# Kernel optimization log

Measured on AMD Instinct MI355X. Metric: run time of the kernel, lower is better.

The kernel has to match this reference:

```python
import jax, jax.numpy as jnp
import numpy as np

B, N, DIM = 1, 4096, 1024
HEADS, DIM_HEAD = 12, 8
POST_LOG_SCALE = 1.0
SCALE = DIM_HEAD ** -0.5


def setup_inputs() -> dict:
    key = jax.random.key(0)
    kx, kw = jax.random.split(key)
    x = jax.random.normal(kx, (B, N, DIM), dtype=jnp.float32)
    # torch nn.Linear(dim, heads*dim_head*2, bias=False) weight: [2*heads*dim_head, dim]
    W = jax.random.normal(kw, (2 * HEADS * DIM_HEAD, DIM), dtype=jnp.float32) * (DIM ** -0.5)
    return {"x": x, "W": W}


def reference(x, W):
    b, n, _ = x.shape
    # linear: x @ W^T -> [b, n, 2*h*d]; rearrange '(qk h d) -> qk b h n d'
    proj = jnp.einsum('bnc,oc->bno', x, W)
    proj = proj.reshape(b, n, 2, HEADS, DIM_HEAD)
    q = jnp.transpose(proj[:, :, 0], (0, 2, 1, 3))  # [b, h, n, d]
    k = jnp.transpose(proj[:, :, 1], (0, 2, 1, 3))  # [b, h, n, d]
    # small-d QK matmul -> [b, h, n, n]
    gates = jnp.einsum('bhid,bhjd->bhij', q, k) * SCALE
    gates = jax.nn.log_sigmoid(gates) * POST_LOG_SCALE
    # causal_mask = triu(ones, diagonal=0); masked_fill -> zero on/above diagonal
    i = jnp.arange(n)[:, None]
    j = jnp.arange(n)[None, :]
    keep = j < i  # strictly lower-triangular entries survive
    gates = jnp.where(keep, gates, 0.0)
    # flip-cumsum-flip == reverse cumulative sum along last axis
    gates = jax.lax.cumsum(gates, axis=3, reverse=True)
    return gates
```

## Files before the change

kernel.cpp:

```cpp
#include <hip/hip_runtime.h>

#define NTOK 4096
#define DIMC 1024
#define HEADS 12
#define DH 8
#define QSCALE 0.35355339059327373f
#define LOG2E  1.4426950408889634f
#define LN2    0.6931471805599453f
#define QPRE   (QSCALE * LOG2E)

typedef float f4 __attribute__((ext_vector_type(4)));
typedef float f2 __attribute__((ext_vector_type(2)));

#define KOFF (HEADS * NTOK * DH)

__global__ __launch_bounds__(256) void k1_proj(const float* __restrict__ x,
                                               const float* __restrict__ W,
                                               float* __restrict__ qk) {
    __shared__ float xs[8 * 1028];
    const int t = threadIdx.x;
    const int row0 = blockIdx.x * 8;

    const f4* x4 = (const f4*)(x + (size_t)row0 * DIMC);
    #pragma unroll
    for (int i = 0; i < 8; ++i) {
        int f = t + i * 256;
        int r = f >> 8;
        int c4 = f & 255;
        f4 v = x4[f];
        *(f4*)(&xs[r * 1028 + c4 * 4]) = v;
    }
    __syncthreads();

    const int g  = t >> 2;
    const int rg = t & 3;

    f2 acc[2][3];
    #pragma unroll
    for (int a = 0; a < 2; ++a)
        #pragma unroll
        for (int m = 0; m < 3; ++m) acc[a][m] = (f2)(0.f);

    const float* w0 = W + (size_t)(3 * g) * DIMC;
    #pragma unroll 2
    for (int c = 0; c < DIMC; c += 4) {
        f4 w[3];
        #pragma unroll
        for (int m = 0; m < 3; ++m)
            w[m] = *(const f4*)(w0 + (size_t)m * DIMC + c);
        #pragma unroll
        for (int a = 0; a < 2; ++a) {
            f4 xv = *(const f4*)(&xs[(rg * 2 + a) * 1028 + c]);
            #pragma unroll
            for (int m = 0; m < 3; ++m) {
                acc[a][m] = __builtin_elementwise_fma(xv.xy, w[m].xy, acc[a][m]);
                acc[a][m] = __builtin_elementwise_fma(xv.zw, w[m].zw, acc[a][m]);
            }
        }
    }

    #pragma unroll
    for (int m = 0; m < 3; ++m) {
        int o   = 3 * g + m;
        int qkf = (o >= 96) ? 1 : 0;
        int oo  = o - 96 * qkf;
        int h   = oo >> 3;
        int d   = oo & 7;
        #pragma unroll
        for (int a = 0; a < 2; ++a) {
            int n = row0 + rg * 2 + a;
            float v = acc[a][m].x + acc[a][m].y;
            if (!qkf) {
                qk[((size_t)h * NTOK + n) * DH + d] = v * QPRE;
            } else {
                qk[KOFF + (((size_t)h * 16 + (n >> 8)) * DH + d) * 256 + (n & 255)] = v;
            }
        }
    }
}

__device__ __forceinline__ float lsig2(float u) {
    float mn = fminf(u, 0.f);
    float z  = __builtin_amdgcn_exp2f(-fabsf(u));
    return mn - __builtin_amdgcn_logf(1.f + z);
}

__global__ __launch_bounds__(256) void k2_gates(const float* __restrict__ qk,
                                                float* __restrict__ out) {
    const int bid  = blockIdx.x;
    const int h    = bid >> 10;
    const int r0   = (bid & 1023) << 2;
    const int t    = threadIdx.x;
    const int lane = t & 63;
    const int w    = t >> 6;
    const int r    = r0 + w;

    __shared__ float ks[2][8 * 256];

    const float* qp = qk + ((size_t)h * NTOK + r) * DH;
    float qs[8];
    #pragma unroll
    for (int d = 0; d < 8; ++d) qs[d] = qp[d];

    float* o = out + ((size_t)h * NTOK + r) * NTOK;
    const int cb = r0 >> 8;
    const int rm = r & 255;

    f4 z = (f4)(0.f);
    for (int cc = 15; cc > cb; --cc)
        __builtin_nontemporal_store(z, (f4*)(o + cc * 256 + 4 * lane));

    {
        const float* kt = qk + KOFF + ((size_t)h * 16 + cb) * 2048;
        f4 a = *(const f4*)(kt + 4 * t);
        f4 b = *(const f4*)(kt + 4 * t + 1024);
        *(f4*)(&ks[0][4 * t]) = a;
        *(f4*)(&ks[0][4 * t + 1024]) = b;
    }
    __syncthreads();

    float carry = 0.f;
    int p = 0;

    for (int c = cb; c >= 0; --c) {
        const int cn = (c > 0) ? (c - 1) : 0;
        const float* kt = qk + KOFF + ((size_t)h * 16 + cn) * 2048;
        f4 sa = *(const f4*)(kt + 4 * t);
        f4 sb = *(const f4*)(kt + 4 * t + 1024);

        f4 kv[8];
        #pragma unroll
        for (int d = 0; d < 8; ++d)
            kv[d] = *(const f4*)(&ks[p][d * 256 + 4 * lane]);

        f2 A = (f2)(0.f), B = (f2)(0.f);
        #pragma unroll
        for (int d = 0; d < 8; ++d) {
            A = __builtin_elementwise_fma(kv[d].xy, (f2)(qs[d]), A);
            B = __builtin_elementwise_fma(kv[d].zw, (f2)(qs[d]), B);
        }

        float g[4];
        if (c == cb) {
            g[0] = (4 * lane + 0 < rm) ? lsig2(A.x) : 0.f;
            g[1] = (4 * lane + 1 < rm) ? lsig2(A.y) : 0.f;
            g[2] = (4 * lane + 2 < rm) ? lsig2(B.x) : 0.f;
            g[3] = (4 * lane + 3 < rm) ? lsig2(B.y) : 0.f;
        } else {
            g[0] = lsig2(A.x); g[1] = lsig2(A.y);
            g[2] = lsig2(B.x); g[3] = lsig2(B.y);
        }

        g[2] += g[3]; g[1] += g[2]; g[0] += g[1];
        const float tot = g[0];
        float s = tot;
        #pragma unroll
        for (int off = 1; off < 64; off <<= 1) {
            float v = __shfl_down(s, off, 64);
            if (lane + off < 64) s += v;
        }
        const float base = (s - tot) + carry;
        carry += __builtin_amdgcn_readfirstlane(s);

        f4 gv = {g[0], g[1], g[2], g[3]};
        __builtin_nontemporal_store((gv + base) * LN2, (f4*)(o + c * 256 + 4 * lane));

        *(f4*)(&ks[p ^ 1][4 * t]) = sa;
        *(f4*)(&ks[p ^ 1][4 * t + 1024]) = sb;
        __syncthreads();
        p ^= 1;
    }
}

extern "C" void kernel_launch(void* const* d_in, const int* in_sizes, int n_in,
                              void* d_out, int out_size, void* d_ws, size_t ws_size,
                              hipStream_t stream) {
    const float* x = (const float*)d_in[0];
    const float* W = (const float*)d_in[1];
    float* out = (float*)d_out;
    float* qk  = (float*)d_ws;

    hipLaunchKernelGGL(k1_proj, dim3(NTOK / 8), dim3(256), 0, stream, x, W, qk);
    hipLaunchKernelGGL(k2_gates, dim3(HEADS * NTOK / 4), dim3(256), 0, stream, qk, out);
}
```

Before: 201.2 us.

## Split gate kernel into segment-totals pass and per-segment scan with tiled stores

```diff
diff --git a/kernel.cpp b/kernel.cpp
--- a/kernel.cpp
+++ b/kernel.cpp
@@ -13,6 +13,7 @@
 typedef float f2 __attribute__((ext_vector_type(2)));
 
 #define KOFF (HEADS * NTOK * DH)
+#define TOFF (2 * KOFF)
 
 __global__ __launch_bounds__(256) void k1_proj(const float* __restrict__ x,
                                                const float* __restrict__ W,
@@ -85,90 +86,123 @@
     return mn - __builtin_amdgcn_logf(1.f + z);
 }
 
-__global__ __launch_bounds__(256) void k2_gates(const float* __restrict__ qk,
-                                                float* __restrict__ out) {
-    const int bid  = blockIdx.x;
-    const int h    = bid >> 10;
-    const int r0   = (bid & 1023) << 2;
+__global__ __launch_bounds__(256) void kA_totals(const float* __restrict__ qk,
+                                                 float* __restrict__ T) {
+    const int blk  = blockIdx.x;
+    const int h    = blk >> 6;
+    const int ib   = blk & 63;
     const int t    = threadIdx.x;
     const int lane = t & 63;
-    const int w    = t >> 6;
-    const int r    = r0 + w;
-
-    __shared__ float ks[2][8 * 256];
+    const int s    = t >> 6;
+    const int i    = ib * 64 + lane;
+
+    const float* qp = qk + ((size_t)h * NTOK + i) * DH;
+    float q[8];
+    #pragma unroll
+    for (int d = 0; d < 8; ++d) q[d] = qp[d];
+
+    float sum = 0.f;
+    const int jlo = s * 1024;
+    int jhi = ib * 64 + 63;
+    if (jhi > jlo + 1024) jhi = jlo + 1024;
+
+    if (jhi > jlo) {
+        for (int j0 = ((jhi - 1) & ~3); j0 >= jlo; j0 -= 4) {
+            const float* kt = qk + KOFF + ((size_t)h * 16 + (j0 >> 8)) * 2048 + (j0 & 255);
+            f2 A = (f2)(0.f), B = (f2)(0.f);
+            #pragma unroll
+            for (int d = 0; d < 8; ++d) {
+                f4 kv = *(const f4*)(kt + d * 256);
+                A = __builtin_elementwise_fma(kv.xy, (f2)(q[d]), A);
+                B = __builtin_elementwise_fma(kv.zw, (f2)(q[d]), B);
+            }
+            float g0 = (j0 + 0 < i) ? lsig2(A.x) : 0.f;
+            float g1 = (j0 + 1 < i) ? lsig2(A.y) : 0.f;
+            float g2 = (j0 + 2 < i) ? lsig2(B.x) : 0.f;
+            float g3 = (j0 + 3 < i) ? lsig2(B.y) : 0.f;
+            sum += g3; sum += g2; sum += g1; sum += g0;
+        }
+    }
+    T[TOFF - TOFF + ((size_t)h * 4 + s) * NTOK + i] = sum;
+}
+
+__global__ __launch_bounds__(64) void kB_gates(const float* __restrict__ qk,
+                                               const float* __restrict__ T,
+                                               float* __restrict__ out) {
+    const int blk  = blockIdx.x;
+    const int s    = blk & 3;
+    const int ib   = (blk >> 2) & 63;
+    const int h    = blk >> 8;
+    const int lane = threadIdx.x;
+    const int r    = ib * 64 + lane;
+
+    __shared__ float tile[64 * 68];
 
     const float* qp = qk + ((size_t)h * NTOK + r) * DH;
-    float qs[8];
-    #pragma unroll
-    for (int d = 0; d < 8; ++d) qs[d] = qp[d];
-
-    float* o = out + ((size_t)h * NTOK + r) * NTOK;
-    const int cb = r0 >> 8;
-    const int rm = r & 255;
-
-    f4 z = (f4)(0.f);
-    for (int cc = 15; cc > cb; --cc)
-        __builtin_nontemporal_store(z, (f4*)(o + cc * 256 + 4 * lane));
-
-    {
-        const float* kt = qk + KOFF + ((size_t)h * 16 + cb) * 2048;
-        f4 a = *(const f4*)(kt + 4 * t);
-        f4 b = *(const f4*)(kt + 4 * t + 1024);
-        *(f4*)(&ks[0][4 * t]) = a;
-        *(f4*)(&ks[0][4 * t + 1024]) = b;
-    }
-    __syncthreads();
+    float q[8];
+    #pragma unroll
+    for (int d = 0; d < 8; ++d) q[d] = qp[d];
 
     float carry = 0.f;
-    int p = 0;
-
-    for (int c = cb; c >= 0; --c) {
-        const int cn = (c > 0) ? (c - 1) : 0;
-        const float* kt = qk + KOFF + ((size_t)h * 16 + cn) * 2048;
-        f4 sa = *(const f4*)(kt + 4 * t);
-        f4 sb = *(const f4*)(kt + 4 * t + 1024);
-
-        f4 kv[8];
-        #pragma unroll
-        for (int d = 0; d < 8; ++d)
-            kv[d] = *(const f4*)(&ks[p][d * 256 + 4 * lane]);
-
-        f2 A = (f2)(0.f), B = (f2)(0.f);
-        #pragma unroll
-        for (int d = 0; d < 8; ++d) {
-            A = __builtin_elementwise_fma(kv[d].xy, (f2)(qs[d]), A);
-            B = __builtin_elementwise_fma(kv[d].zw, (f2)(qs[d]), B);
-        }
-
-        float g[4];
-        if (c == cb) {
-            g[0] = (4 * lane + 0 < rm) ? lsig2(A.x) : 0.f;
-            g[1] = (4 * lane + 1 < rm) ? lsig2(A.y) : 0.f;
-            g[2] = (4 * lane + 2 < rm) ? lsig2(B.x) : 0.f;
-            g[3] = (4 * lane + 3 < rm) ? lsig2(B.y) : 0.f;
+    #pragma unroll
+    for (int s2 = 3; s2 >= 1; --s2)
+        if (s2 > s) carry += T[((size_t)h * 4 + s2) * NTOK + r];
+
+    float* orow0 = out + ((size_t)h * NTOK + ib * 64) * NTOK;
+    const f4 z = (f4)(0.f);
+
+    for (int jb = s * 16 + 15; jb >= s * 16; --jb) {
+        if (jb > ib) {
+            #pragma unroll
+            for (int rr = 0; rr < 16; ++rr) {
+                int row = rr * 4 + (lane >> 4);
+                int c4  = (lane & 15) * 4;
+                __builtin_nontemporal_store(z,
+                    (f4*)(orow0 + (size_t)row * NTOK + jb * 64 + c4));
+            }
         } else {
-            g[0] = lsig2(A.x); g[1] = lsig2(A.y);
-            g[2] = lsig2(B.x); g[3] = lsig2(B.y);
-        }
-
-        g[2] += g[3]; g[1] += g[2]; g[0] += g[1];
-        const float tot = g[0];
-        float s = tot;
-        #pragma unroll
-        for (int off = 1; off < 64; off <<= 1) {
-            float v = __shfl_down(s, off, 64);
-            if (lane + off < 64) s += v;
-        }
-        const float base = (s - tot) + carry;
-        carry += __builtin_amdgcn_readfirstlane(s);
-
-        f4 gv = {g[0], g[1], g[2], g[3]};
-        __builtin_nontemporal_store((gv + base) * LN2, (f4*)(o + c * 256 + 4 * lane));
-
-        *(f4*)(&ks[p ^ 1][4 * t]) = sa;
-        *(f4*)(&ks[p ^ 1][4 * t + 1024]) = sb;
-        __syncthreads();
-        p ^= 1;
+            const bool diag = (jb == ib);
+            const float* kt = qk + KOFF + ((size_t)h * 16 + (jb >> 2)) * 2048 + (jb & 3) * 64;
+
+            for (int jf = 15; jf >= 0; --jf) {
+                const int j0 = jb * 64 + jf * 4;
+                const float* kp = kt + jf * 4;
+                f2 A = (f2)(0.f), B = (f2)(0.f);
+                #pragma unroll
+                for (int d = 0; d < 8; ++d) {
+                    f4 kv = *(const f4*)(kp + d * 256);
+                    A = __builtin_elementwise_fma(kv.xy, (f2)(q[d]), A);
+                    B = __builtin_elementwise_fma(kv.zw, (f2)(q[d]), B);
+                }
+                float g0, g1, g2, g3;
+                if (diag) {
+                    g0 = (j0 + 0 < r) ? lsig2(A.x) : 0.f;
+                    g1 = (j0 + 1 < r) ? lsig2(A.y) : 0.f;
+                    g2 = (j0 + 2 < r) ? lsig2(B.x) : 0.f;
+                    g3 = (j0 + 3 < r) ? lsig2(B.y) : 0.f;
+                } else {
+                    g0 = lsig2(A.x); g1 = lsig2(A.y);
+                    g2 = lsig2(B.x); g3 = lsig2(B.y);
+                }
+                float v3 = g3 + carry;
+                float v2 = g2 + v3;
+                float v1 = g1 + v2;
+                float v0 = g0 + v1;
+                carry = v0;
+                f4 v = {v0 * LN2, v1 * LN2, v2 * LN2, v3 * LN2};
+                *(f4*)(&tile[lane * 68 + jf * 4]) = v;
+            }
+            __syncthreads();
+            #pragma unroll
+            for (int rr = 0; rr < 16; ++rr) {
+                int row = rr * 4 + (lane >> 4);
+                int c4  = (lane & 15) * 4;
+                f4 v = *(const f4*)(&tile[row * 68 + c4]);
+                __builtin_nontemporal_store(v,
+                    (f4*)(orow0 + (size_t)row * NTOK + jb * 64 + c4));
+            }
+            __syncthreads();
+        }
     }
 }
 
@@ -179,7 +213,9 @@
     const float* W = (const float*)d_in[1];
     float* out = (float*)d_out;
     float* qk  = (float*)d_ws;
+    float* T   = qk + TOFF;
 
     hipLaunchKernelGGL(k1_proj, dim3(NTOK / 8), dim3(256), 0, stream, x, W, qk);
-    hipLaunchKernelGGL(k2_gates, dim3(HEADS * NTOK / 4), dim3(256), 0, stream, qk, out);
-}
+    hipLaunchKernelGGL(kA_totals, dim3(HEADS * 64), dim3(256), 0, stream, qk, T);
+    hipLaunchKernelGGL(kB_gates, dim3(HEADS * 64 * 4), dim3(64), 0, stream, qk, T, out);
+}
```

After: 470.6 us. +133.8%, slower.

## Drop LDS K staging in gates kernel, read K from global, batch stores

Applied to the files above, without the earlier changes.

```diff
diff --git a/kernel.cpp b/kernel.cpp
--- a/kernel.cpp
+++ b/kernel.cpp
@@ -85,90 +85,87 @@
     return mn - __builtin_amdgcn_logf(1.f + z);
 }
 
-__global__ __launch_bounds__(256) void k2_gates(const float* __restrict__ qk,
+__global__ __launch_bounds__(512) void k2_gates(const float* __restrict__ qk,
                                                 float* __restrict__ out) {
     const int bid  = blockIdx.x;
-    const int h    = bid >> 10;
-    const int r0   = (bid & 1023) << 2;
+    const int h    = bid >> 9;
+    const int i0   = (bid & 511) << 3;
     const int t    = threadIdx.x;
     const int lane = t & 63;
-    const int w    = t >> 6;
-    const int r    = r0 + w;
-
-    __shared__ float ks[2][8 * 256];
+    const int wid  = t >> 6;
+    const int r    = i0 + wid;
 
     const float* qp = qk + ((size_t)h * NTOK + r) * DH;
-    float qs[8];
+    float q[8];
     #pragma unroll
-    for (int d = 0; d < 8; ++d) qs[d] = qp[d];
+    for (int d = 0; d < 8; ++d) q[d] = qp[d];
 
+    const float* kh = qk + KOFF + (size_t)h * (16 * DH * 256) + 4 * lane;
     float* o = out + ((size_t)h * NTOK + r) * NTOK;
-    const int cb = r0 >> 8;
-    const int rm = r & 255;
 
-    f4 z = (f4)(0.f);
-    for (int cc = 15; cc > cb; --cc)
-        __builtin_nontemporal_store(z, (f4*)(o + cc * 256 + 4 * lane));
+    const int cb = r >> 8;
+    const int bb = cb >> 2;
 
-    {
-        const float* kt = qk + KOFF + ((size_t)h * 16 + cb) * 2048;
-        f4 a = *(const f4*)(kt + 4 * t);
-        f4 b = *(const f4*)(kt + 4 * t + 1024);
-        *(f4*)(&ks[0][4 * t]) = a;
-        *(f4*)(&ks[0][4 * t + 1024]) = b;
+    const f4 z = (f4)(0.f);
+
+    for (int b = 3; b > bb; --b) {
+        float* ob = o + b * 1024 + 4 * lane;
+        #pragma unroll
+        for (int sub = 0; sub < 4; ++sub)
+            __builtin_nontemporal_store(z, (f4*)(ob + sub * 256));
     }
-    __syncthreads();
 
     float carry = 0.f;
-    int p = 0;
+    for (int b = bb; b >= 0; --b) {
+        f4 ov[4];
+        #pragma unroll
+        for (int sub = 3; sub >= 0; --sub) {
+            const int cc = b * 4 + sub;
+            if (cc > cb) { ov[sub] = z; continue; }
 
-    for (int c = cb; c >= 0; --c) {
-        const int cn = (c > 0) ? (c - 1) : 0;
-        const float* kt = qk + KOFF + ((size_t)h * 16 + cn) * 2048;
-        f4 sa = *(const f4*)(kt + 4 * t);
-        f4 sb = *(const f4*)(kt + 4 * t + 1024);
+            const float* kc = kh + (size_t)cc * 2048;
+            f4 kv[8];
+            #pragma unroll
+            for (int d = 0; d < 8; ++d) kv[d] = *(const f4*)(kc + d * 256);
 
-        f4 kv[8];
-        #pragma unroll
-        for (int d = 0; d < 8; ++d)
-            kv[d] = *(const f4*)(&ks[p][d * 256 + 4 * lane]);
+            f2 A = (f2)(0.f), B = (f2)(0.f);
+            #pragma unroll
+            for (int d = 0; d < 8; ++d) {
+                A = __builtin_elementwise_fma(kv[d].xy, (f2)(q[d]), A);
+                B = __builtin_elementwise_fma(kv[d].zw, (f2)(q[d]), B);
+            }
 
-        f2 A = (f2)(0.f), B = (f2)(0.f);
-        #pragma unroll
-        for (int d = 0; d < 8; ++d) {
-            A = __builtin_elementwise_fma(kv[d].xy, (f2)(qs[d]), A);
-            B = __builtin_elementwise_fma(kv[d].zw, (f2)(qs[d]), B);
+            const int j0 = cc * 256 + 4 * lane;
+            float g0, g1, g2, g3;
+            if (cc == cb) {
+                g0 = (j0 + 0 < r) ? lsig2(A.x) : 0.f;
+                g1 = (j0 + 1 < r) ? lsig2(A.y) : 0.f;
+                g2 = (j0 + 2 < r) ? lsig2(B.x) : 0.f;
+                g3 = (j0 + 3 < r) ? lsig2(B.y) : 0.f;
+            } else {
+                g0 = lsig2(A.x); g1 = lsig2(A.y);
+                g2 = lsig2(B.x); g3 = lsig2(B.y);
+            }
+
+            g2 += g3; g1 += g2; g0 += g1;
+            const float tot = g0;
+            float s = tot;
+            #pragma unroll
+            for (int off = 1; off < 64; off <<= 1) {
+                float v = __shfl_down(s, off, 64);
+                if (lane + off < 64) s += v;
+            }
+            const float base = (s - tot) + carry;
+            carry += __builtin_amdgcn_readfirstlane(s);
+
+            f4 gv = {g0, g1, g2, g3};
+            ov[sub] = (gv + base) * LN2;
         }
 
-        float g[4];
-        if (c == cb) {
-            g[0] = (4 * lane + 0 < rm) ? lsig2(A.x) : 0.f;
-            g[1] = (4 * lane + 1 < rm) ? lsig2(A.y) : 0.f;
-            g[2] = (4 * lane + 2 < rm) ? lsig2(B.x) : 0.f;
-            g[3] = (4 * lane + 3 < rm) ? lsig2(B.y) : 0.f;
-        } else {
-            g[0] = lsig2(A.x); g[1] = lsig2(A.y);
-            g[2] = lsig2(B.x); g[3] = lsig2(B.y);
-        }
-
-        g[2] += g[3]; g[1] += g[2]; g[0] += g[1];
-        const float tot = g[0];
-        float s = tot;
+        float* ob = o + b * 1024 + 4 * lane;
         #pragma unroll
-        for (int off = 1; off < 64; off <<= 1) {
-            float v = __shfl_down(s, off, 64);
-            if (lane + off < 64) s += v;
-        }
-        const float base = (s - tot) + carry;
-        carry += __builtin_amdgcn_readfirstlane(s);
-
-        f4 gv = {g[0], g[1], g[2], g[3]};
-        __builtin_nontemporal_store((gv + base) * LN2, (f4*)(o + c * 256 + 4 * lane));
-
-        *(f4*)(&ks[p ^ 1][4 * t]) = sa;
-        *(f4*)(&ks[p ^ 1][4 * t + 1024]) = sb;
-        __syncthreads();
-        p ^= 1;
+        for (int sub = 0; sub < 4; ++sub)
+            __builtin_nontemporal_store(ov[sub], (f4*)(ob + sub * 256));
     }
 }
 
@@ -181,5 +178,5 @@
     float* qk  = (float*)d_ws;
 
     hipLaunchKernelGGL(k1_proj, dim3(NTOK / 8), dim3(256), 0, stream, x, W, qk);
-    hipLaunchKernelGGL(k2_gates, dim3(HEADS * NTOK / 4), dim3(256), 0, stream, qk, out);
+    hipLaunchKernelGGL(k2_gates, dim3(HEADS * NTOK / 8), dim3(512), 0, stream, qk, out);
 }
```

New measurement: 204.1 us. Within noise of the previous version (+1.4%).
